# Kernel optimization log

Measured on AMD Instinct MI355X. Metric: run time of the kernel, lower is better.

The kernel has to match this reference:

```python
import jax, jax.numpy as jnp
import numpy as np


def setup_inputs() -> dict:
    key = jax.random.key(0)
    ks = jax.random.split(key, 7)
    B, N, F, H = 128, 64, 128, 128
    s1 = 1.0 / np.sqrt(2 * N)  # torch Linear default-ish scaling
    s2 = 1.0 / np.sqrt(H)
    return {
        "agent_features": jax.random.normal(ks[0], (B, N, F), dtype=jnp.float32),
        "W1": jax.random.normal(ks[1], (2 * N, H), dtype=jnp.float32) * s1,
        "b1": jax.random.normal(ks[2], (H,), dtype=jnp.float32) * s1,
        "W2": jax.random.normal(ks[3], (H, H), dtype=jnp.float32) * s2,
        "b2": jax.random.normal(ks[4], (H,), dtype=jnp.float32) * s2,
        "w3": jax.random.normal(ks[5], (H,), dtype=jnp.float32) * s2,
        "b3": jax.random.normal(ks[6], (1,), dtype=jnp.float32) * s2,
        "mixing_weights": jnp.ones((N,), dtype=jnp.float32) / N,
    }


def reference(agent_features, W1, b1, W2, b2, w3, b3, mixing_weights):
    N = mixing_weights.shape[0]
    f = agent_features[:, :, :N]  # [B, N, N] (first num_agents features)
    # Split first Linear's weight into the i-half and j-half of the concat:
    # concat([f_i, f_j]) @ W1 == f_i @ W1[:N] + f_j @ W1[N:]
    Ai = jnp.einsum('bnf,fh->bnh', f, W1[:N])   # contribution of agent i
    Aj = jnp.einsum('bnf,fh->bnh', f, W1[N:])   # contribution of agent j
    h1 = jax.nn.relu(Ai[:, :, None, :] + Aj[:, None, :, :] + b1)  # [B,N,N,H]
    h2 = jax.nn.relu(jnp.einsum('bijh,hk->bijk', h1, W2) + b2)    # [B,N,N,H]
    correlations = jax.nn.sigmoid(jnp.einsum('bijh,h->bij', h2, w3) + b3[0])
    weights = jax.nn.softmax(mixing_weights, axis=0)
    return correlations, weights
```

## Files before the change

### kernel.cpp

```cpp
#include <hip/hip_runtime.h>
#include <hip/hip_bf16.h>


typedef __bf16 bf16x8 __attribute__((ext_vector_type(8)));
typedef float f32x4 __attribute__((ext_vector_type(4)));

#define B_SZ 128
#define N_SZ 64
#define H_SZ 128

__device__ __forceinline__ unsigned pack_bf16x2(float lo, float hi) {
  unsigned a = __float_as_uint(lo);
  unsigned b = __float_as_uint(hi);
  a += 0x7fffu + ((a >> 16) & 1u);
  b += 0x7fffu + ((b >> 16) & 1u);
  return (a >> 16) | (b & 0xffff0000u);
}

__global__ __launch_bounds__(256) void setup_kernel(
    const float* __restrict__ af, const float* __restrict__ W1,
    const float* __restrict__ b1, const float* __restrict__ W2,
    const float* __restrict__ mw, float* __restrict__ AiP,
    float* __restrict__ Aj, unsigned short* __restrict__ W2T,
    float* __restrict__ outw)
{
  const int blk = blockIdx.x;
  const int tid = threadIdx.x;

  if (blk < 2048) {
    __shared__ float fl[4 * 64];
    const int bn0 = blk << 2;
    fl[tid] = af[((bn0 + (tid >> 6)) << 7) + (tid & 63)];
    __syncthreads();
    const int h    = tid & 127;
    const int half = tid >> 7;
    const float* Wp = W1 + ((half << 6) << 7) + h;
    float acc0 = 0.f, acc1 = 0.f, acc2 = 0.f, acc3 = 0.f;
#pragma unroll
    for (int fq = 0; fq < 16; ++fq) {
      const float w0 = Wp[(fq * 4 + 0) << 7];
      const float w1v = Wp[(fq * 4 + 1) << 7];
      const float w2v = Wp[(fq * 4 + 2) << 7];
      const float w3v = Wp[(fq * 4 + 3) << 7];
      const float4 f0 = *(const float4*)&fl[0 * 64 + (fq << 2)];
      const float4 f1 = *(const float4*)&fl[1 * 64 + (fq << 2)];
      const float4 f2 = *(const float4*)&fl[2 * 64 + (fq << 2)];
      const float4 f3 = *(const float4*)&fl[3 * 64 + (fq << 2)];
      acc0 = fmaf(f0.x, w0, fmaf(f0.y, w1v, fmaf(f0.z, w2v, fmaf(f0.w, w3v, acc0))));
      acc1 = fmaf(f1.x, w0, fmaf(f1.y, w1v, fmaf(f1.z, w2v, fmaf(f1.w, w3v, acc1))));
      acc2 = fmaf(f2.x, w0, fmaf(f2.y, w1v, fmaf(f2.z, w2v, fmaf(f2.w, w3v, acc2))));
      acc3 = fmaf(f3.x, w0, fmaf(f3.y, w1v, fmaf(f3.z, w2v, fmaf(f3.w, w3v, acc3))));
    }
    if (half == 0) {
      const float bb = b1[h];
      AiP[((bn0 + 0) << 7) + h] = acc0 + bb;
      AiP[((bn0 + 1) << 7) + h] = acc1 + bb;
      AiP[((bn0 + 2) << 7) + h] = acc2 + bb;
      AiP[((bn0 + 3) << 7) + h] = acc3 + bb;
    } else {
      Aj[((bn0 + 0) << 7) + h] = acc0;
      Aj[((bn0 + 1) << 7) + h] = acc1;
      Aj[((bn0 + 2) << 7) + h] = acc2;
      Aj[((bn0 + 3) << 7) + h] = acc3;
    }
  } else if (blk < 2112) {
    int idx = ((blk - 2048) << 8) + tid;
    int k = idx >> 7, n = idx & 127;
    unsigned u = __float_as_uint(W2[idx]);
    u += 0x7fffu + ((u >> 16) & 1u);
    W2T[(n << 7) + k] = (unsigned short)(u >> 16);
  } else {
    if (tid < 64) {
      float v = mw[tid];
      float m = v;
      for (int off = 32; off > 0; off >>= 1) m = fmaxf(m, __shfl_xor(m, off));
      float e = expf(v - m);
      float s = e;
      for (int off = 32; off > 0; off >>= 1) s += __shfl_xor(s, off);
      outw[tid] = e / s;
    }
  }
}

__global__ __launch_bounds__(512, 4) void corr_kernel(
    const float* __restrict__ AiP, const float* __restrict__ Aj,
    const unsigned short* __restrict__ W2T,
    const float* __restrict__ b2, const float* __restrict__ w3,
    const float* __restrict__ b3, float* __restrict__ out)
{
  __shared__ __align__(16) unsigned short W2s[128 * 128];
  __shared__ __align__(16) unsigned short At[128 * 128];
  __shared__ float part[256];

  const int tid  = threadIdx.x;
  const int lane = tid & 63;
  const int wave = tid >> 6;
  const int c = lane & 15, g = lane >> 4;
  const int wm = wave & 1;
  const int wn = wave >> 1;

  const int blk = blockIdx.x;
  const int b   = blk >> 2;
  const int ip0 = (blk & 3) << 3;

  {
    const uint4* src = (const uint4*)W2T;
#pragma unroll
    for (int it = 0; it < 4; ++it) {
      const int idx = (it << 9) + tid;
      const int n = idx >> 4, e = idx & 15;
      const uint4 v = src[idx];
      *(uint4*)&W2s[(n << 7) + ((e ^ (n & 15)) << 3)] = v;
    }
  }

  f32x4 b2v[4], w3v[4];
#pragma unroll
  for (int tm = 0; tm < 4; ++tm) {
    b2v[tm] = *(const f32x4*)(b2 + (wm << 6) + (tm << 4) + (g << 2));
    w3v[tm] = *(const f32x4*)(w3 + (wm << 6) + (tm << 4) + (g << 2));
  }
  const float bias3 = b3[0];

  const float* AjB = Aj + ((b << 6) << 7);

  const int kq = tid & 31;
  const int rr = tid >> 5;
  const int be = kq >> 1, hf = kq & 1;

  for (int t = 0; t < 8; ++t) {
    const int i0 = (ip0 + t) << 1;
    const float* AiB = AiP + (((b << 6) + i0) << 7);

    __syncthreads();

#pragma unroll
    for (int pass = 0; pass < 8; ++pass) {
      const int r = (pass << 4) + rr;
      const float4 a4 = ((const float4*)(AiB + ((r >> 6) << 7)))[kq];
      const float4 c4 = ((const float4*)(AjB + ((r & 63) << 7)))[kq];
      uint2 val;
      val.x = pack_bf16x2(fmaxf(a4.x + c4.x, 0.f), fmaxf(a4.y + c4.y, 0.f));
      val.y = pack_bf16x2(fmaxf(a4.z + c4.z, 0.f), fmaxf(a4.w + c4.w, 0.f));
      *(uint2*)&At[(r << 7) + ((be ^ (r & 15)) << 3) + (hf << 2)] = val;
    }

    __syncthreads();

    f32x4 acc[4][2];
#pragma unroll
    for (int tm = 0; tm < 4; ++tm) {
      acc[tm][0] = b2v[tm];
      acc[tm][1] = b2v[tm];
    }

#pragma unroll
    for (int kt = 0; kt < 4; ++kt) {
      const int es = ((kt << 2) + g) ^ c;
      bf16x8 wv[4], hv[2];
#pragma unroll
      for (int tm = 0; tm < 4; ++tm)
        wv[tm] = *(const bf16x8*)&W2s[(((wm << 6) + (tm << 4) + c) << 7) + (es << 3)];
#pragma unroll
      for (int tn = 0; tn < 2; ++tn)
        hv[tn] = *(const bf16x8*)&At[(((wn << 5) + (tn << 4) + c) << 7) + (es << 3)];
#pragma unroll
      for (int tm = 0; tm < 4; ++tm)
#pragma unroll
        for (int tn = 0; tn < 2; ++tn)
          acc[tm][tn] = __builtin_amdgcn_mfma_f32_16x16x32_bf16(
              wv[tm], hv[tn], acc[tm][tn], 0, 0, 0);
    }

    float s0 = 0.f, s1 = 0.f;
#pragma unroll
    for (int tm = 0; tm < 4; ++tm) {
#pragma unroll
      for (int p = 0; p < 4; ++p) {
        s0 = fmaf(fmaxf(acc[tm][0][p], 0.f), w3v[tm][p], s0);
        s1 = fmaf(fmaxf(acc[tm][1][p], 0.f), w3v[tm][p], s1);
      }
    }
    s0 += __shfl_xor(s0, 16);
    s0 += __shfl_xor(s0, 32);
    s1 += __shfl_xor(s1, 16);
    s1 += __shfl_xor(s1, 32);
    if (g == 0) {
      part[(((wn << 5) + c) << 1) + wm]      = s0;
      part[(((wn << 5) + 16 + c) << 1) + wm] = s1;
    }

    __syncthreads();

    if (tid < 128) {
      const float2 pp = *(const float2*)&part[tid << 1];
      const float v = pp.x + pp.y + bias3;
      out[(b << 12) + (i0 << 6) + tid] = 1.f / (1.f + __expf(-v));
    }
  }
}

extern "C" void kernel_launch(void* const* d_in, const int* in_sizes, int n_in,
                              void* d_out, int out_size, void* d_ws,
                              size_t ws_size, hipStream_t stream)
{
  const float* af = (const float*)d_in[0];
  const float* W1 = (const float*)d_in[1];
  const float* b1 = (const float*)d_in[2];
  const float* W2 = (const float*)d_in[3];
  const float* b2 = (const float*)d_in[4];
  const float* w3 = (const float*)d_in[5];
  const float* b3 = (const float*)d_in[6];
  const float* mw = (const float*)d_in[7];
  float* out = (float*)d_out;

  float* AiP = (float*)d_ws;
  float* Aj  = AiP + B_SZ * N_SZ * H_SZ;
  unsigned short* W2T = (unsigned short*)(Aj + B_SZ * N_SZ * H_SZ);

  setup_kernel<<<2113, 256, 0, stream>>>(af, W1, b1, W2, mw, AiP, Aj, W2T,
                                         out + B_SZ * N_SZ * N_SZ);
  corr_kernel<<<512, 512, 0, stream>>>(AiP, Aj, W2T, b2, w3, b3, out);
}
```

Baseline: 104.1 us.

## Keep W2 in registers and build h1 fragments on the fly from LDS

The kernel now holds its W2 slice in registers as MFMA operand fragments instead of staging W2 in shared memory. Aj for the batch and the block's Ai rows are staged once into padded fp32 shared arrays, so each wave forms relu(Ai+Aj) bf16 fragments directly in registers rather than materialising a bf16 h1 tile in LDS. A double-buffered partial-sum array cuts the loop from three barriers per iteration to one. This removes per-iteration global reloads and LDS round trips, at the cost of more register pressure and redundant add/convert work across waves that share rows.

```diff
diff --git a/kernel.cpp b/kernel.cpp
--- a/kernel.cpp
+++ b/kernel.cpp
@@ -8,14 +8,6 @@
 #define B_SZ 128
 #define N_SZ 64
 #define H_SZ 128
-
-__device__ __forceinline__ unsigned pack_bf16x2(float lo, float hi) {
-  unsigned a = __float_as_uint(lo);
-  unsigned b = __float_as_uint(hi);
-  a += 0x7fffu + ((a >> 16) & 1u);
-  b += 0x7fffu + ((b >> 16) & 1u);
-  return (a >> 16) | (b & 0xffff0000u);
-}
 
 __global__ __launch_bounds__(256) void setup_kernel(
     const float* __restrict__ af, const float* __restrict__ W1,
@@ -88,9 +80,10 @@
     const float* __restrict__ b2, const float* __restrict__ w3,
     const float* __restrict__ b3, float* __restrict__ out)
 {
-  __shared__ __align__(16) unsigned short W2s[128 * 128];
-  __shared__ __align__(16) unsigned short At[128 * 128];
-  __shared__ float part[256];
+  __shared__ __align__(16) float AjF[64 * 132];
+  __shared__ __align__(16) float AiF[16 * 132];
+  __shared__ float b2s[128], w3s[128];
+  __shared__ float part[2][2][128];
 
   const int tid  = threadIdx.x;
   const int lane = tid & 63;
@@ -104,98 +97,96 @@
   const int ip0 = (blk & 3) << 3;
 
   {
-    const uint4* src = (const uint4*)W2T;
-#pragma unroll
-    for (int it = 0; it < 4; ++it) {
-      const int idx = (it << 9) + tid;
-      const int n = idx >> 4, e = idx & 15;
-      const uint4 v = src[idx];
-      *(uint4*)&W2s[(n << 7) + ((e ^ (n & 15)) << 3)] = v;
-    }
+    const float4* src = (const float4*)(Aj + (b << 13));
+#pragma unroll
+    for (int p = 0; p < 4; ++p) {
+      const int idx = (p << 9) + tid;
+      const int r = idx >> 5, u = idx & 31;
+      *(float4*)&AjF[r * 132 + (u << 2)] = src[idx];
+    }
+    const float4* srcA = (const float4*)(AiP + (((b << 6) + (ip0 << 1)) << 7));
+    {
+      const int r = tid >> 5, u = tid & 31;
+      *(float4*)&AiF[r * 132 + (u << 2)] = srcA[tid];
+    }
+    if (tid < 128) b2s[tid] = b2[tid];
+    else if (tid < 256) w3s[tid - 128] = w3[tid - 128];
   }
 
-  f32x4 b2v[4], w3v[4];
-#pragma unroll
-  for (int tm = 0; tm < 4; ++tm) {
-    b2v[tm] = *(const f32x4*)(b2 + (wm << 6) + (tm << 4) + (g << 2));
-    w3v[tm] = *(const f32x4*)(w3 + (wm << 6) + (tm << 4) + (g << 2));
-  }
+  bf16x8 w2r[4][4];
+#pragma unroll
+  for (int mt = 0; mt < 4; ++mt)
+#pragma unroll
+    for (int kt = 0; kt < 4; ++kt)
+      w2r[mt][kt] = *(const bf16x8*)&W2T[(((wm << 6) + (mt << 4) + c) << 7) +
+                                         (kt << 5) + (g << 3)];
   const float bias3 = b3[0];
 
-  const float* AjB = Aj + ((b << 6) << 7);
-
-  const int kq = tid & 31;
-  const int rr = tid >> 5;
-  const int be = kq >> 1, hf = kq & 1;
+  const int j0 = ((wn << 5) + c) & 63;
+  const int j1 = ((wn << 5) + 16 + c) & 63;
+  const float* ajb0 = &AjF[j0 * 132 + (g << 3)];
+  const float* ajb1 = &AjF[j1 * 132 + (g << 3)];
+  const int i_sel = wn >> 1;
+
+  __syncthreads();
 
   for (int t = 0; t < 8; ++t) {
-    const int i0 = (ip0 + t) << 1;
-    const float* AiB = AiP + (((b << 6) + i0) << 7);
+    const float* aib = &AiF[((t << 1) + i_sel) * 132 + (g << 3)];
+    float s[2];
+
+#pragma unroll
+    for (int tn = 0; tn < 2; ++tn) {
+      const float* ajb = tn ? ajb1 : ajb0;
+
+      f32x4 acc[4];
+#pragma unroll
+      for (int mt = 0; mt < 4; ++mt)
+        acc[mt] = *(const f32x4*)&b2s[(wm << 6) + (mt << 4) + (g << 2)];
+
+#pragma unroll
+      for (int kt = 0; kt < 4; ++kt) {
+        const f32x4 a0 = *(const f32x4*)(aib + (kt << 5));
+        const f32x4 a1 = *(const f32x4*)(aib + (kt << 5) + 4);
+        const f32x4 c0 = *(const f32x4*)(ajb + (kt << 5));
+        const f32x4 c1 = *(const f32x4*)(ajb + (kt << 5) + 4);
+        f32x4 h0 = a0 + c0;
+        f32x4 h1v = a1 + c1;
+        bf16x8 hv;
+#pragma unroll
+        for (int e = 0; e < 4; ++e) {
+          hv[e]     = (__bf16)fmaxf(h0[e], 0.f);
+          hv[e + 4] = (__bf16)fmaxf(h1v[e], 0.f);
+        }
+#pragma unroll
+        for (int mt = 0; mt < 4; ++mt)
+          acc[mt] = __builtin_amdgcn_mfma_f32_16x16x32_bf16(
+              w2r[mt][kt], hv, acc[mt], 0, 0, 0);
+      }
+
+      float sv = 0.f;
+#pragma unroll
+      for (int mt = 0; mt < 4; ++mt) {
+        const f32x4 wv3 = *(const f32x4*)&w3s[(wm << 6) + (mt << 4) + (g << 2)];
+#pragma unroll
+        for (int p = 0; p < 4; ++p)
+          sv = fmaf(fmaxf(acc[mt][p], 0.f), wv3[p], sv);
+      }
+      sv += __shfl_xor(sv, 16);
+      sv += __shfl_xor(sv, 32);
+      s[tn] = sv;
+    }
+
+    const int pb = t & 1;
+    if (g == 0) {
+      part[pb][wm][(wn << 5) + c]      = s[0];
+      part[pb][wm][(wn << 5) + 16 + c] = s[1];
+    }
 
     __syncthreads();
 
-#pragma unroll
-    for (int pass = 0; pass < 8; ++pass) {
-      const int r = (pass << 4) + rr;
-      const float4 a4 = ((const float4*)(AiB + ((r >> 6) << 7)))[kq];
-      const float4 c4 = ((const float4*)(AjB + ((r & 63) << 7)))[kq];
-      uint2 val;
-      val.x = pack_bf16x2(fmaxf(a4.x + c4.x, 0.f), fmaxf(a4.y + c4.y, 0.f));
-      val.y = pack_bf16x2(fmaxf(a4.z + c4.z, 0.f), fmaxf(a4.w + c4.w, 0.f));
-      *(uint2*)&At[(r << 7) + ((be ^ (r & 15)) << 3) + (hf << 2)] = val;
-    }
-
-    __syncthreads();
-
-    f32x4 acc[4][2];
-#pragma unroll
-    for (int tm = 0; tm < 4; ++tm) {
-      acc[tm][0] = b2v[tm];
-      acc[tm][1] = b2v[tm];
-    }
-
-#pragma unroll
-    for (int kt = 0; kt < 4; ++kt) {
-      const int es = ((kt << 2) + g) ^ c;
-      bf16x8 wv[4], hv[2];
-#pragma unroll
-      for (int tm = 0; tm < 4; ++tm)
-        wv[tm] = *(const bf16x8*)&W2s[(((wm << 6) + (tm << 4) + c) << 7) + (es << 3)];
-#pragma unroll
-      for (int tn = 0; tn < 2; ++tn)
-        hv[tn] = *(const bf16x8*)&At[(((wn << 5) + (tn << 4) + c) << 7) + (es << 3)];
-#pragma unroll
-      for (int tm = 0; tm < 4; ++tm)
-#pragma unroll
-        for (int tn = 0; tn < 2; ++tn)
-          acc[tm][tn] = __builtin_amdgcn_mfma_f32_16x16x32_bf16(
-              wv[tm], hv[tn], acc[tm][tn], 0, 0, 0);
-    }
-
-    float s0 = 0.f, s1 = 0.f;
-#pragma unroll
-    for (int tm = 0; tm < 4; ++tm) {
-#pragma unroll
-      for (int p = 0; p < 4; ++p) {
-        s0 = fmaf(fmaxf(acc[tm][0][p], 0.f), w3v[tm][p], s0);
-        s1 = fmaf(fmaxf(acc[tm][1][p], 0.f), w3v[tm][p], s1);
-      }
-    }
-    s0 += __shfl_xor(s0, 16);
-    s0 += __shfl_xor(s0, 32);
-    s1 += __shfl_xor(s1, 16);
-    s1 += __shfl_xor(s1, 32);
-    if (g == 0) {
-      part[(((wn << 5) + c) << 1) + wm]      = s0;
-      part[(((wn << 5) + 16 + c) << 1) + wm] = s1;
-    }
-
-    __syncthreads();
-
     if (tid < 128) {
-      const float2 pp = *(const float2*)&part[tid << 1];
-      const float v = pp.x + pp.y + bias3;
-      out[(b << 12) + (i0 << 6) + tid] = 1.f / (1.f + __expf(-v));
+      const float v = part[pb][0][tid] + part[pb][1][tid] + bias3;
+      out[(b << 12) + ((ip0 + t) << 7) + tid] = 1.f / (1.f + __expf(-v));
     }
   }
 }
```

New measurement: 184.0 us. 76.7% more time.
